# Performance work log

Measured on AMD Instinct MI355X. Metric: run time of the kernel, lower is better.

The kernel has to match this reference:

```python
import jax, jax.numpy as jnp
import numpy as np
import math

B, C, H, W = 8, 384, 14, 14
HEADS = 12
HC = C // HEADS
STRIDE = 2
K = 3
FACTOR = 2.0
rH = -(-H // STRIDE)
rW = -(-W // STRIDE)
N = H * W
S = rH * rW
KK = K * K
OFFSET_MAT = np.array([[0, -1], [-1, -1], [-1, 0], [-1, 1], [0, 1], [1, 1], [1, 0], [1, -1], [0, 0]], dtype=np.float32)


def bilinear_sample(img, coords):
    """img (Hi,Wi,C); coords (...,2) normalized (y,x) in [-1,1].
    Matches F.grid_sample(mode='bilinear', align_corners=True, padding_mode='zeros')."""
    Hi, Wi = img.shape[0], img.shape[1]
    py = (coords[..., 0] + 1.0) * 0.5 * (Hi - 1)
    px = (coords[..., 1] + 1.0) * 0.5 * (Wi - 1)
    y0 = jnp.floor(py)
    x0 = jnp.floor(px)
    wy1 = py - y0
    wx1 = px - x0

    def corner(yf, xf, wgt):
        valid = (yf >= 0) & (yf <= Hi - 1) & (xf >= 0) & (xf <= Wi - 1)
        yi = jnp.clip(yf, 0, Hi - 1).astype(jnp.int32)
        xi = jnp.clip(xf, 0, Wi - 1).astype(jnp.int32)
        return img[yi, xi] * (wgt * valid)[..., None]

    return (corner(y0, x0, (1 - wy1) * (1 - wx1)) + corner(y0, x0 + 1, (1 - wy1) * wx1)
            + corner(y0 + 1, x0, wy1 * (1 - wx1)) + corner(y0 + 1, x0 + 1, wy1 * wx1))


def _forward(x, Wq, bq, Wk, bk, Wv, bv, Wo1, bo1, Wdw, bdw, ln_g, ln_b, Wo2, Wco, posembed, Wp, bp):
    dt = x.dtype
    xh = jnp.transpose(x, (0, 2, 3, 1))                       # B,H,W,C
    q = jnp.einsum('bhwc,oc->bhwo', xh, Wq) + bq              # q_conv (1x1)

    # ---- offset network: 1x1 conv -> GELU -> 3x3 dw stride conv -> LN -> GELU -> 1x1 ----
    t = jax.nn.gelu(jnp.einsum('bhwc,oc->bhwo', q, Wo1) + bo1, approximate=False)
    ker = jnp.transpose(Wdw, (2, 3, 1, 0))                    # (3,3,1,C) for HWIO depthwise
    t = jax.lax.conv_general_dilated(t, ker, (STRIDE, STRIDE), ((1, 1), (1, 1)),
                                     dimension_numbers=('NHWC', 'HWIO', 'NHWC'),
                                     feature_group_count=C) + bdw  # B,rH,rW,C
    mu = t.mean(-1, keepdims=True)
    var = ((t - mu) ** 2).mean(-1, keepdims=True)
    t = (t - mu) / jnp.sqrt(var + 1e-5) * ln_g + ln_b
    t = jax.nn.gelu(t, approximate=False)
    off = jnp.einsum('bhwc,oc->bhwo', t, Wo2)                 # B,rH,rW,2*N ; channel = (g,h,w)
    off = off.reshape(B, rH, rW, 2, N)
    off = jnp.transpose(off, (0, 3, 4, 1, 2))                 # B,2,N,rH,rW
    ranges = jnp.array([1.0 / H, 1.0 / W], dtype=dt)
    off = jnp.tanh(off) * ranges[None, :, None, None, None] * FACTOR
    off = jnp.transpose(off, (0, 2, 3, 4, 1))                 # B,N,rH,rW,2 (y,x)

    # ---- strided reference grid + deformable bilinear gather from x ----
    gy = jnp.arange(0, H, STRIDE, dtype=dt) / (H - 1) * 2 - 1
    gx = jnp.arange(0, W, STRIDE, dtype=dt) / (W - 1) * 2 - 1
    ref = jnp.stack(jnp.meshgrid(gy, gx, indexing='ij'), -1)  # rH,rW,2
    dpos = off + ref
    sampled = jax.vmap(bilinear_sample)(xh, dpos).reshape(B, N, S, C)

    # ---- k x k center points with learned offsets ----
    cy = jnp.arange(H, dtype=dt)
    cx = jnp.arange(W, dtype=dt)
    center = jnp.stack(jnp.meshgrid(cy, cx, indexing='ij'), -1).reshape(N, 1, 2)
    offmat = jnp.asarray(OFFSET_MAT, dtype=dt)
    cpt = center + offmat[None]                               # N,KK,2
    cpt_norm = jnp.stack([jnp.clip(cpt[..., 0], 0, H) / (H - 1) * 2 - 1,
                          jnp.clip(cpt[..., 1], 0, W) / (W - 1) * 2 - 1], -1).reshape(N, K, K, 2)
    q_tok = q.reshape(B, N, C)
    co = jnp.tanh(jnp.einsum('bnc,oc->bno', q_tok, Wco).reshape(B, N, K, K, 2)) * ranges
    cgrid = co + cpt_norm[None]
    csampled = jax.vmap(bilinear_sample)(xh, cgrid).reshape(B, N, KK, C)

    feats = jnp.concatenate([sampled, csampled], axis=2)      # B,N,S+KK,C
    k = (jnp.einsum('bnsc,oc->bnso', feats, Wk) + bk).reshape(B, N, S + KK, HEADS, HC)
    v = (jnp.einsum('bnsc,oc->bnso', feats, Wv) + bv).reshape(B, N, S + KK, HEADS, HC)
    qh = q_tok.reshape(B, N, HEADS, HC)
    attn = jnp.einsum('bnhd,bnshd->bhns', qh, k)              # qk_scale=None -> no scaling

    # ---- dynamic relative position bias (grid_sample into rel-pos table) ----
    a = jnp.arange(0, H, STRIDE, dtype=dt)
    bcol = jnp.arange(0, W, dtype=dt)
    ref_pos = a[None, :] - bcol[:, None]                      # (W, rH)
    ref_pos_x = jnp.tile(ref_pos, (H, rH))                    # (N, S)
    ref_pos_y = jnp.repeat(jnp.repeat(ref_pos, W, axis=0), rW, axis=1)
    rpp = jnp.stack([ref_pos_y / (H - 1), ref_pos_x / (W - 1)], -1)  # N,S,2
    rel = rpp.reshape(N, rH, rW, 2)[None] - off               # B,N,rH,rW,2
    table = jnp.transpose(posembed, (1, 2, 0))                # (2H-1, 2W-1, heads)
    d_rel = bilinear_sample(table, rel).reshape(B, N, S, HEADS)
    cpt_raw = jnp.broadcast_to(center, (N, KK, 2)).reshape(N, K, K, 2)
    crel = co - cpt_raw[None]
    d_crel = bilinear_sample(table, crel).reshape(B, N, KK, HEADS)
    bias = jnp.concatenate([d_rel, d_crel], axis=2)           # B,N,S+KK,heads
    attn = attn + jnp.transpose(bias, (0, 3, 1, 2))
    attn = jax.nn.softmax(attn, axis=-1)

    out = jnp.einsum('bhns,bnshd->bnhd', attn, v).reshape(B, N, C)
    out = jnp.einsum('bnc,oc->bno', out, Wp) + bp             # proj (1x1)
    return jnp.transpose(out.reshape(B, H, W, C), (0, 3, 1, 2))


def setup_inputs() -> dict:
    key = jax.random.key(0)
    ks = jax.random.split(key, 20)
    def w(k, shape, s=0.05):
        return jax.random.normal(k, shape, dtype=jnp.float32) * s
    return {
        'x': jax.random.normal(ks[0], (B, C, H, W), dtype=jnp.float32),
        'Wq': w(ks[1], (C, C)), 'bq': w(ks[2], (C,)),
        'Wk': w(ks[3], (C, C)), 'bk': w(ks[4], (C,)),
        'Wv': w(ks[5], (C, C)), 'bv': w(ks[6], (C,)),
        'Wo1': w(ks[7], (C, C)), 'bo1': w(ks[8], (C,)),
        'Wdw': w(ks[9], (C, 1, 3, 3), 0.2), 'bdw': w(ks[10], (C,)),
        'ln_g': jnp.ones((C,), jnp.float32), 'ln_b': jnp.zeros((C,), jnp.float32),
        'Wo2': w(ks[11], (2 * N, C)),
        'Wco': w(ks[12], (2 * K * K, C)),
        'posembed': w(ks[13], (HEADS, 2 * H - 1, 2 * W - 1), 0.02),
        'Wp': w(ks[14], (C, C)), 'bp': w(ks[15], (C,)),
    }


def reference(x, Wq, bq, Wk, bk, Wv, bv, Wo1, bo1, Wdw, bdw, ln_g, ln_b, Wo2, Wco, posembed, Wp, bp):
    return _forward(x, Wq, bq, Wk, bk, Wv, bv, Wo1, bo1, Wdw, bdw, ln_g, ln_b, Wo2, Wco, posembed, Wp, bp)
```

## Files before the change

### kernel.cpp

```cpp
#include <hip/hip_runtime.h>
#include <hip/hip_bf16.h>
#include <math.h>

#define BB 8
#define CC 384
#define HH 14
#define WW 14
#define NHEADS 12
#define RH 7
#define RW 7
#define NN 196
#define SS 49
#define KKK 9
#define SK 58
#define TH 27
#define NTOK 1568
#define WSZ 147456
#define WO2SZ 150528

typedef float    f4 __attribute__((ext_vector_type(4)));
typedef _Float16 h8 __attribute__((ext_vector_type(8)));
typedef _Float16 h4 __attribute__((ext_vector_type(4)));

__device__ __forceinline__ float geluf(float x){ return 0.5f*x*(1.0f+erff(x*0.7071067811865475f)); }
__device__ __forceinline__ f4 mfma16h(h8 a, h8 b, f4 c){
  return __builtin_amdgcn_mfma_f32_16x16x32_f16(a, b, c, 0, 0, 0);
}

__constant__ float c_offm[9][2] = {{0,-1},{-1,-1},{-1,0},{-1,1},{0,1},{1,1},{1,0},{1,-1},{0,0}};

__global__ void __launch_bounds__(256) k_pre(const float* __restrict__ x,
    _Float16* __restrict__ xhh, _Float16* __restrict__ xlo,
    const float* __restrict__ Wq, const float* __restrict__ Wk, const float* __restrict__ Wo1,
    const float* __restrict__ Wp, const float* __restrict__ Wv, const float* __restrict__ Wo2,
    _Float16* __restrict__ Wh, _Float16* __restrict__ Wl){
  __shared__ float tile[48*203];
  int bid = blockIdx.x;
  int t = threadIdx.x;
  if (bid < 64){
    int b = bid >> 3, c0 = (bid & 7)*48;
    for (int i = t; i < 48*49; i += 256){
      int row = i / 49, seg = i % 49;
      f4 v = *(const f4*)(x + ((size_t)(b*CC + c0 + row))*NN + seg*4);
      #pragma unroll
      for (int j = 0; j < 4; ++j) tile[row*203 + seg*4 + j] = v[j];
    }
    __syncthreads();
    for (int i = t; i < 196*12; i += 256){
      int n = i / 12, seg = i % 12;
      h4 vh, vl;
      #pragma unroll
      for (int j = 0; j < 4; ++j){
        float v = tile[(seg*4 + j)*203 + n];
        vh[j] = (_Float16)v;
        vl[j] = (_Float16)(v - (float)vh[j]);
      }
      size_t o = ((size_t)(b*NN + n))*CC + c0 + seg*4;
      *(h4*)(xhh + o) = vh;
      *(h4*)(xlo + o) = vl;
    }
  } else if (bid < 424){
    int bid2 = bid - 64;
    int mat = bid2 / 72;
    int e0 = (bid2 % 72)*2048 + t*8;
    const float* src = mat==0?Wq: mat==1?Wk: mat==2?Wo1: mat==3?Wp: Wv;
    f4 v0 = *(const f4*)(src + e0);
    f4 v1 = *(const f4*)(src + e0 + 4);
    h8 hi, lo;
    #pragma unroll
    for (int j = 0; j < 4; ++j){
      hi[j]   = (_Float16)v0[j]; lo[j]   = (_Float16)(v0[j] - (float)hi[j]);
      hi[4+j] = (_Float16)v1[j]; lo[4+j] = (_Float16)(v1[j] - (float)hi[4+j]);
    }
    *(h8*)(Wh + (size_t)mat*WSZ + e0) = hi;
    *(h8*)(Wl + (size_t)mat*WSZ + e0) = lo;
  } else {
    int e0 = (bid - 424)*2048 + t*8;
    if (e0 < WO2SZ){
      f4 v0 = *(const f4*)(Wo2 + e0);
      f4 v1 = *(const f4*)(Wo2 + e0 + 4);
      h8 hi, lo;
      #pragma unroll
      for (int j = 0; j < 4; ++j){
        hi[j]   = (_Float16)v0[j]; lo[j]   = (_Float16)(v0[j] - (float)hi[j]);
        hi[4+j] = (_Float16)v1[j]; lo[4+j] = (_Float16)(v1[j] - (float)hi[4+j]);
      }
      *(h8*)(Wh + (size_t)5*WSZ + e0) = hi;
      *(h8*)(Wl + (size_t)5*WSZ + e0) = lo;
    }
  }
}

__device__ __forceinline__ void gemm_pre_body(
    const _Float16* __restrict__ Ahg, const _Float16* __restrict__ Alg,
    const _Float16* __restrict__ Bhg, const _Float16* __restrict__ Blg,
    int arow, int brow, _Float16* sbuf, int t, f4 acc[4]){
  _Float16* Ah = sbuf; _Float16* Al = sbuf + 2560;
  _Float16* Bh = sbuf + 5120; _Float16* Bl = sbuf + 7680;
  int w = t>>6, lane = t&63, col = lane&15, quad = lane>>4;
  int r = t>>2, cg = t&3;
  const _Float16* Arh = Ahg + (size_t)arow*384 + cg*8;
  const _Float16* Arl = Alg + (size_t)arow*384 + cg*8;
  const _Float16* Brh = Bhg + (size_t)brow*384 + cg*8;
  const _Float16* Brl = Blg + (size_t)brow*384 + cg*8;
  h8 ah = *(const h8*)(Arh), al = *(const h8*)(Arl);
  h8 bh = *(const h8*)(Brh), bl = *(const h8*)(Brl);
  for (int k0 = 0; k0 < 384; k0 += 32){
    __syncthreads();
    *(h8*)(Ah + r*40 + cg*8) = ah; *(h8*)(Al + r*40 + cg*8) = al;
    *(h8*)(Bh + r*40 + cg*8) = bh; *(h8*)(Bl + r*40 + cg*8) = bl;
    __syncthreads();
    if (k0 < 352){
      ah = *(const h8*)(Arh + k0 + 32); al = *(const h8*)(Arl + k0 + 32);
      bh = *(const h8*)(Brh + k0 + 32); bl = *(const h8*)(Brl + k0 + 32);
    }
    h8 afh = *(const h8*)(Ah + (w*16+col)*40 + quad*8);
    h8 afl = *(const h8*)(Al + (w*16+col)*40 + quad*8);
    #pragma unroll
    for (int nt = 0; nt < 4; ++nt){
      h8 bfh = *(const h8*)(Bh + (nt*16+col)*40 + quad*8);
      h8 bfl = *(const h8*)(Bl + (nt*16+col)*40 + quad*8);
      acc[nt] = mfma16h(afh, bfh, acc[nt]);
      acc[nt] = mfma16h(afl, bfh, acc[nt]);
      acc[nt] = mfma16h(afh, bfl, acc[nt]);
    }
  }
}

__global__ void __launch_bounds__(256) k_qkv(
    const _Float16* __restrict__ xhh, const _Float16* __restrict__ xlo,
    const _Float16* __restrict__ Wh, const _Float16* __restrict__ Wl,
    const float* __restrict__ bq,
    float* __restrict__ qf, _Float16* __restrict__ qfh, _Float16* __restrict__ qfl,
    _Float16* __restrict__ K2h, _Float16* __restrict__ VprojT){
  __shared__ __align__(16) _Float16 sbuf[10240];
  int t = threadIdx.x;
  int w = t>>6, lane = t&63, col = lane&15, quad = lane>>4;
  int bid = blockIdx.x;

  if (bid < 300){
    int isK = (bid >= 150) ? 1 : 0;
    int r2 = isK ? bid - 150 : bid;
    const _Float16* Bh = Wh + (size_t)(isK ? 1 : 0)*WSZ;
    const _Float16* Bl = Wl + (size_t)(isK ? 1 : 0)*WSZ;
    int m0 = (r2/6)*64, n0 = (r2%6)*64;
    int r = t>>2;
    int arow = min(m0 + r, NTOK-1);
    int brow = n0 + r;
    f4 acc[4] = {{0,0,0,0},{0,0,0,0},{0,0,0,0},{0,0,0,0}};
    gemm_pre_body(xhh, xlo, Bh, Bl, arow, brow, sbuf, t, acc);
    #pragma unroll
    for (int nt = 0; nt < 4; ++nt){
      #pragma unroll
      for (int rr = 0; rr < 4; ++rr){
        int m = m0 + w*16 + quad*4 + rr;
        int o = n0 + nt*16 + col;
        if (m >= NTOK) continue;
        if (isK){
          K2h[(size_t)m*384 + o] = (_Float16)acc[nt][rr];
        } else {
          float v = acc[nt][rr] + bq[o];
          qf[(size_t)m*384 + o] = v;
          _Float16 vh = (_Float16)v;
          qfh[(size_t)m*384 + o] = vh;
          qfl[(size_t)m*384 + o] = (_Float16)(v - (float)vh);
        }
      }
    }
  } else {
    int idx = bid - 300;
    int mo = idx % 6;
    int ny = (idx / 6) % 4;
    int b  = idx / 24;
    int m0 = mo*64, n0 = ny*64;
    int orow = m0 + w*16 + col;
    const _Float16* wvh = Wh + (size_t)4*WSZ + (size_t)orow*384;
    const _Float16* wvl = Wl + (size_t)4*WSZ + (size_t)orow*384;
    f4 acc[4] = {{0,0,0,0},{0,0,0,0},{0,0,0,0},{0,0,0,0}};
    for (int kt = 0; kt < 12; ++kt){
      h8 ah = *(const h8*)(wvh + kt*32 + quad*8);
      h8 al = *(const h8*)(wvl + kt*32 + quad*8);
      #pragma unroll
      for (int nt = 0; nt < 4; ++nt){
        int i = min(n0 + nt*16 + col, 195);
        h8 b8 = *(const h8*)(xhh + ((size_t)(b*196 + i))*384 + kt*32 + quad*8);
        acc[nt] = mfma16h(ah, b8, acc[nt]);
        acc[nt] = mfma16h(al, b8, acc[nt]);
      }
    }
    #pragma unroll
    for (int nt = 0; nt < 4; ++nt){
      #pragma unroll
      for (int rr = 0; rr < 4; ++rr){
        int o = m0 + w*16 + quad*4 + rr;
        int i = n0 + nt*16 + col;
        if (i < 224)
          VprojT[((size_t)(b*384 + o))*224 + i] = (i < 196) ? (_Float16)acc[nt][rr] : (_Float16)0.f;
      }
    }
  }
}

__global__ void __launch_bounds__(256) k_mid(
    const _Float16* __restrict__ qfh, const _Float16* __restrict__ qfl,
    const _Float16* __restrict__ Wh, const _Float16* __restrict__ Wl,
    const float* __restrict__ bo1, float* __restrict__ t1,
    const _Float16* __restrict__ K2h, _Float16* __restrict__ G16){
  __shared__ __align__(16) _Float16 sbuf[10240];
  int t = threadIdx.x;
  int w = t>>6, lane = t&63, col = lane&15, quad = lane>>4;
  int bid = blockIdx.x;
  if (bid < 150){
    const _Float16* Bh = Wh + (size_t)2*WSZ;
    const _Float16* Bl = Wl + (size_t)2*WSZ;
    int m0 = (bid/6)*64, n0 = (bid%6)*64;
    int r = t>>2;
    int arow = min(m0 + r, NTOK-1);
    int brow = n0 + r;
    f4 acc[4] = {{0,0,0,0},{0,0,0,0},{0,0,0,0},{0,0,0,0}};
    gemm_pre_body(qfh, qfl, Bh, Bl, arow, brow, sbuf, t, acc);
    #pragma unroll
    for (int nt = 0; nt < 4; ++nt){
      #pragma unroll
      for (int rr = 0; rr < 4; ++rr){
        int m = m0 + w*16 + quad*4 + rr;
        int o = n0 + nt*16 + col;
        if (m >= NTOK) continue;
        t1[(size_t)m*384 + o] = geluf(acc[nt][rr] + bo1[o]);
      }
    }
  } else {
    int idx = bid - 150;
    int m0 = (idx & 3)*64;
    int bh = idx >> 2; int b = bh / 12, h = bh - b*12;
    const _Float16* qr = qfh + ((size_t)(b*196 + min(m0 + w*16 + col, 195)))*384 + h*32;
    h8 a8 = *(const h8*)(qr + quad*8);
    f4 acc[13];
    #pragma unroll
    for (int nt = 0; nt < 13; ++nt){
      int i = min(nt*16 + col, 195);
      h8 b8 = *(const h8*)(K2h + ((size_t)(b*196 + i))*384 + h*32 + quad*8);
      f4 z = {0.f,0.f,0.f,0.f};
      acc[nt] = mfma16h(a8, b8, z);
    }
    #pragma unroll
    for (int nt = 0; nt < 13; ++nt){
      #pragma unroll
      for (int r = 0; r < 4; ++r){
        int m = m0 + w*16 + quad*4 + r;
        int i = nt*16 + col;
        if (m < 196 && i < 196)
          G16[((size_t)(b*196 + m))*2352 + h*196 + i] = (_Float16)acc[nt][r];
      }
    }
  }
}

__global__ void __launch_bounds__(384) k_dwln(const float* __restrict__ t1,
      const float* __restrict__ Wdw, const float* __restrict__ bdw,
      const float* __restrict__ lng, const float* __restrict__ lnb,
      _Float16* __restrict__ t2h, _Float16* __restrict__ t2l){
  int blk = blockIdx.x;
  int ow = blk % RW; int oh = (blk / RW) % RH; int b = blk / (RH*RW);
  int c = threadIdx.x;
  float acc = bdw[c];
  #pragma unroll
  for (int kh = 0; kh < 3; ++kh){
    int ih = oh*2 - 1 + kh;
    if (ih < 0 || ih >= HH) continue;
    #pragma unroll
    for (int kw = 0; kw < 3; ++kw){
      int iw = ow*2 - 1 + kw;
      if (iw < 0 || iw >= WW) continue;
      acc += t1[((b*HH + ih)*WW + iw)*CC + c] * Wdw[c*9 + kh*3 + kw];
    }
  }
  __shared__ float red[6];
  __shared__ float s_mu, s_rv;
  float v = acc;
  #pragma unroll
  for (int o = 32; o > 0; o >>= 1) v += __shfl_down(v, o);
  int wid = c >> 6, lane = c & 63;
  if (lane == 0) red[wid] = v;
  __syncthreads();
  if (c == 0){ float s = 0.f; for (int i = 0; i < 6; ++i) s += red[i]; s_mu = s / CC; }
  __syncthreads();
  float mu = s_mu;
  float d = acc - mu;
  v = d*d;
  #pragma unroll
  for (int o = 32; o > 0; o >>= 1) v += __shfl_down(v, o);
  if (lane == 0) red[wid] = v;
  __syncthreads();
  if (c == 0){ float s = 0.f; for (int i = 0; i < 6; ++i) s += red[i]; s_rv = rsqrtf(s / CC + 1e-5f); }
  __syncthreads();
  float val = geluf(d * s_rv * lng[c] + lnb[c]);
  _Float16 vh = (_Float16)val;
  t2h[blk*CC + c] = vh;
  t2l[blk*CC + c] = (_Float16)(val - (float)vh);
}

__global__ void __launch_bounds__(256) k_off(
    const _Float16* __restrict__ t2h, const _Float16* __restrict__ t2l,
    const _Float16* __restrict__ Wh, const _Float16* __restrict__ Wl,
    float* __restrict__ offp){
  __shared__ __align__(16) _Float16 sbuf[10240];
  int t = threadIdx.x;
  int w = t>>6, lane = t&63, col = lane&15, quad = lane>>4;
  int bid = blockIdx.x;
  int m0 = (bid/7)*64, n0 = (bid%7)*64;
  int r = t>>2;
  int arow = min(m0 + r, 391);
  int brow = min(n0 + r, 391);
  const _Float16* Bh = Wh + (size_t)5*WSZ;
  const _Float16* Bl = Wl + (size_t)5*WSZ;
  f4 acc[4] = {{0,0,0,0},{0,0,0,0},{0,0,0,0},{0,0,0,0}};
  gemm_pre_body(t2h, t2l, Bh, Bl, arow, brow, sbuf, t, acc);
  #pragma unroll
  for (int nt = 0; nt < 4; ++nt){
    #pragma unroll
    for (int rr = 0; rr < 4; ++rr){
      int row = m0 + w*16 + quad*4 + rr;
      int o = n0 + nt*16 + col;
      if (row < 392 && o < 392){
        int g = o / NN, nn = o % NN;
        int b = row / SS, s = row % SS;
        float rng = (g == 0) ? (1.0f/HH) : (1.0f/WW);
        offp[((b*NN + nn)*SS + s)*2 + g] = tanhf(acc[nt][rr]) * rng * 2.0f;
      }
    }
  }
}

__global__ void __launch_bounds__(256, 7) k_fused(
    const float* __restrict__ qf, const float* __restrict__ off,
    const _Float16* __restrict__ G16,
    const float* __restrict__ bk, const float* __restrict__ Wco, const float* __restrict__ pos,
    _Float16* __restrict__ agg16){
  __shared__ __align__(16) _Float16 Gs[2352];
  __shared__ __align__(16) float agg[12*228];
  __shared__ float scoreS[696];
  __shared__ float offl[98];
  __shared__ float colb[18];
  __shared__ float qbv[12];
  __shared__ uint2 tapv[232];
  float* qrow = agg;

  int blk = blockIdx.x;
  int n = blk % NN, b = blk / NN;
  int iy = n / WW, ix = n % WW;
  int t = threadIdx.x;

  {
    const h8* g8 = (const h8*)(G16 + (size_t)blk*2352);
    h8* gs8 = (h8*)Gs;
    for (int i = t; i < 294; i += 256) gs8[i] = g8[i];
  }
  {
    const f4* q4 = (const f4*)(qf + (size_t)blk*384);
    f4* qr4 = (f4*)qrow;
    for (int i = t; i < 96; i += 256) qr4[i] = q4[i];
  }
  for (int i = t; i < 98; i += 256) offl[i] = off[(size_t)blk*98 + i];
  __syncthreads();

  if (t < 144){
    int o = t >> 3, l = t & 7;
    const float* wr = Wco + o*384 + l*48;
    const float* qr = qrow + l*48;
    f4 a4 = {0.f,0.f,0.f,0.f};
    #pragma unroll
    for (int c = 0; c < 48; c += 4) a4 += (*(const f4*)(qr + c)) * (*(const f4*)(wr + c));
    float acc = a4[0]+a4[1]+a4[2]+a4[3];
    acc += __shfl_xor(acc, 1); acc += __shfl_xor(acc, 2); acc += __shfl_xor(acc, 4);
    if (l == 0){
      int g = o & 1;
      float range = (g == 0) ? (1.0f/HH) : (1.0f/WW);
      colb[o] = tanhf(acc) * range;
    }
  }
  if (t >= 160){
    int o = t - 160;
    int h = o >> 3, l = o & 7;
    float acc = 0.f;
    for (int d = l; d < 32; d += 8) acc += qrow[h*32 + d] * bk[h*32 + d];
    acc += __shfl_xor(acc, 1); acc += __shfl_xor(acc, 2); acc += __shfl_xor(acc, 4);
    if (l == 0 && h < 12) qbv[h] = acc;
  }
  __syncthreads();

  if (t < SK){
    float cy, cx;
    if (t < SS){
      int sy = t / RW, sx = t % RW;
      cy = offl[t*2+0] + ((2.0f*sy)/13.0f*2.0f - 1.0f);
      cx = offl[t*2+1] + ((2.0f*sx)/13.0f*2.0f - 1.0f);
    } else {
      int kk = t - SS;
      float cyr = fminf(fmaxf((float)iy + c_offm[kk][0], 0.f), (float)HH);
      float cxr = fminf(fmaxf((float)ix + c_offm[kk][1], 0.f), (float)WW);
      cy = colb[kk*2+0] + (cyr/13.0f*2.0f - 1.0f);
      cx = colb[kk*2+1] + (cxr/13.0f*2.0f - 1.0f);
    }
    float py = (cy + 1.0f)*0.5f*13.0f;
    float px = (cx + 1.0f)*0.5f*13.0f;
    float y0 = floorf(py), x0 = floorf(px);
    float wy1 = py - y0, wx1 = px - x0;
    #pragma unroll
    for (int k4 = 0; k4 < 4; ++k4){
      float yf = y0 + (k4 >> 1), xf = x0 + (k4 & 1);
      bool valid = (yf >= 0.f) && (yf <= 13.f) && (xf >= 0.f) && (xf <= 13.f);
      int yi = (int)fminf(fmaxf(yf, 0.f), 13.f);
      int xi = (int)fminf(fmaxf(xf, 0.f), 13.f);
      float wgt = ((k4 >> 1) ? wy1 : (1.f - wy1)) * ((k4 & 1) ? wx1 : (1.f - wx1));
      tapv[t*4 + k4] = make_uint2(__float_as_uint(valid ? wgt : 0.f),
                                  (unsigned)(yi*WW + xi));
    }
  }
  __syncthreads();
  for (int i = t; i < 12*228; i += 256) agg[i] = 0.f;

  if (t < 232){
    int s = t >> 2, grp = t & 3;
    float ry, rx;
    if (s < SS){
      int sy = s / RW, sx = s % RW;
      ry = (2.0f*sy - iy)/13.0f - offl[s*2+0];
      rx = (2.0f*sx - ix)/13.0f - offl[s*2+1];
    } else {
      int kk = s - SS;
      ry = colb[kk*2+0] - (float)iy;
      rx = colb[kk*2+1] - (float)ix;
    }
    float py = (ry + 1.0f)*0.5f*26.0f;
    float px = (rx + 1.0f)*0.5f*26.0f;
    float y0 = floorf(py), x0 = floorf(px);
    float wy1 = py - y0, wx1 = px - x0;
    int pidx[4]; float pw[4];
    #pragma unroll
    for (int k4 = 0; k4 < 4; ++k4){
      float yf = y0 + (k4 >> 1), xf = x0 + (k4 & 1);
      bool valid = (yf >= 0.f) && (yf <= 26.f) && (xf >= 0.f) && (xf <= 26.f);
      int yi = (int)fminf(fmaxf(yf, 0.f), 26.f);
      int xi = (int)fminf(fmaxf(xf, 0.f), 26.f);
      pidx[k4] = yi*TH + xi;
      float wgt = ((k4 >> 1) ? wy1 : (1.f - wy1)) * ((k4 & 1) ? wx1 : (1.f - wx1));
      pw[k4] = valid ? wgt : 0.f;
    }
    uint2 tp0 = tapv[s*4+0], tp1 = tapv[s*4+1], tp2 = tapv[s*4+2], tp3 = tapv[s*4+3];
    float tw0 = __uint_as_float(tp0.x), tw1 = __uint_as_float(tp1.x);
    float tw2 = __uint_as_float(tp2.x), tw3 = __uint_as_float(tp3.x);
    #pragma unroll
    for (int hh = 0; hh < 3; ++hh){
      int h = grp*3 + hh;
      const float* pt = pos + h*729;
      float val = qbv[h];
      val += pt[pidx[0]]*pw[0];
      val += pt[pidx[1]]*pw[1];
      val += pt[pidx[2]]*pw[2];
      val += pt[pidx[3]]*pw[3];
      const _Float16* gh = Gs + h*196;
      val += tw0*(float)gh[(int)tp0.y];
      val += tw1*(float)gh[(int)tp1.y];
      val += tw2*(float)gh[(int)tp2.y];
      val += tw3*(float)gh[(int)tp3.y];
      scoreS[h*58 + s] = val;
    }
  }
  __syncthreads();

  if (t < 192){
    int h = t >> 4, l = t & 15;
    float v[4];
    #pragma unroll
    for (int k = 0; k < 4; ++k){ int s = l + 16*k; v[k] = (s < SK) ? scoreS[h*58 + s] : -1e30f; }
    float mx = fmaxf(fmaxf(v[0], v[1]), fmaxf(v[2], v[3]));
    mx = fmaxf(mx, __shfl_xor(mx, 1)); mx = fmaxf(mx, __shfl_xor(mx, 2));
    mx = fmaxf(mx, __shfl_xor(mx, 4)); mx = fmaxf(mx, __shfl_xor(mx, 8));
    float e[4], sum = 0.f;
    #pragma unroll
    for (int k = 0; k < 4; ++k){ int s = l + 16*k; e[k] = (s < SK) ? expf(v[k] - mx) : 0.f; sum += e[k]; }
    sum += __shfl_xor(sum, 1); sum += __shfl_xor(sum, 2);
    sum += __shfl_xor(sum, 4); sum += __shfl_xor(sum, 8);
    float inv = 1.0f / sum;
    #pragma unroll
    for (int k = 0; k < 4; ++k){
      int s = l + 16*k;
      if (s < SK) scoreS[h*58 + s] = e[k]*inv;
    }
  }
  __syncthreads();

  if (t < 232){
    uint2 tp = tapv[t];
    float wv = __uint_as_float(tp.x);
    if (wv != 0.f){
      int s = t >> 2, cell = (int)tp.y;
      float* ag = agg + cell;
      #pragma unroll
      for (int h = 0; h < 12; ++h)
        atomicAdd(ag + h*228, scoreS[h*58 + s]*wv);
    }
  }
  __syncthreads();

  {
    _Float16* ar = agg16 + (size_t)blk*2688;
    for (int i = t; i < 336; i += 256){
      int d = i*8;
      int h = d / 224, j = d - h*224;
      const float* src = agg + h*228 + j;
      f4 a = *(const f4*)src;
      f4 c = *(const f4*)(src + 4);
      h8 o;
      #pragma unroll
      for (int k = 0; k < 4; ++k){ o[k] = (_Float16)a[k]; o[4+k] = (_Float16)c[k]; }
      *(h8*)(ar + d) = o;
    }
  }
}

__global__ void __launch_bounds__(256) k_av(const _Float16* __restrict__ agg16,
                                            const _Float16* __restrict__ VprojT,
                                            const float* __restrict__ bv,
                                            _Float16* __restrict__ otokh, _Float16* __restrict__ otokl){
  int t = threadIdx.x;
  int w = t>>6, lane = t&63, col = lane&15, quad = lane>>4;
  int m0 = blockIdx.x*64;
  int bh = blockIdx.y; int b = bh / 12, h = bh - b*12;
  const _Float16* ar = agg16 + ((size_t)(b*196 + min(m0 + w*16 + col, 195)))*2688 + h*224;
  f4 acc[2] = {{0,0,0,0},{0,0,0,0}};
  for (int kt = 0; kt < 7; ++kt){
    h8 a8 = *(const h8*)(ar + kt*32 + quad*8);
    #pragma unroll
    for (int nt = 0; nt < 2; ++nt){
      int o = h*32 + nt*16 + col;
      h8 b8 = *(const h8*)(VprojT + ((size_t)(b*384 + o))*224 + kt*32 + quad*8);
      acc[nt] = mfma16h(a8, b8, acc[nt]);
    }
  }
  #pragma unroll
  for (int nt = 0; nt < 2; ++nt){
    #pragma unroll
    for (int rr = 0; rr < 4; ++rr){
      int m = m0 + w*16 + quad*4 + rr;
      if (m < 196){
        int o = h*32 + nt*16 + col;
        float v = acc[nt][rr] + bv[o];
        size_t idx = ((size_t)(b*196 + m))*384 + o;
        _Float16 vh = (_Float16)v;
        otokh[idx] = vh;
        otokl[idx] = (_Float16)(v - (float)vh);
      }
    }
  }
}

__global__ void __launch_bounds__(256) k_proj(
    const _Float16* __restrict__ otokh, const _Float16* __restrict__ otokl,
    const _Float16* __restrict__ Wh, const _Float16* __restrict__ Wl,
    const float* __restrict__ bias, float* __restrict__ out){
  __shared__ __align__(16) _Float16 sbuf[10240];
  int t = threadIdx.x;
  int w = t>>6, lane = t&63, col = lane&15, quad = lane>>4;
  int m0 = blockIdx.x*64, n0 = blockIdx.y*64;
  int r = t>>2;
  int arow = min(m0 + r, NTOK-1);
  int brow = n0 + r;
  const _Float16* Bh = Wh + (size_t)3*WSZ;
  const _Float16* Bl = Wl + (size_t)3*WSZ;
  f4 acc[4] = {{0,0,0,0},{0,0,0,0},{0,0,0,0},{0,0,0,0}};
  gemm_pre_body(otokh, otokl, Bh, Bl, arow, brow, sbuf, t, acc);
  float* tile = (float*)sbuf;
  __syncthreads();
  #pragma unroll
  for (int nt = 0; nt < 4; ++nt)
    #pragma unroll
    for (int rr = 0; rr < 4; ++rr)
      tile[(w*16 + quad*4 + rr)*65 + nt*16 + col] = acc[nt][rr];
  __syncthreads();
  for (int i = t; i < 1024; i += 256){
    int o_l = i >> 4, ms = i & 15;
    int m = m0 + ms*4;
    if (m >= NTOK) continue;
    int bb = m / NN, nnn = m % NN;
    int o = n0 + o_l;
    float bo = bias[o];
    f4 v = { tile[(ms*4+0)*65 + o_l] + bo, tile[(ms*4+1)*65 + o_l] + bo,
             tile[(ms*4+2)*65 + o_l] + bo, tile[(ms*4+3)*65 + o_l] + bo };
    *(f4*)(out + ((size_t)bb*384 + o)*NN + nnn) = v;
  }
}

extern "C" void kernel_launch(void* const* d_in, const int* in_sizes, int n_in,
                              void* d_out, int out_size, void* d_ws, size_t ws_size,
                              hipStream_t stream){
  const float* x    = (const float*)d_in[0];
  const float* Wq   = (const float*)d_in[1];
  const float* bq   = (const float*)d_in[2];
  const float* Wk   = (const float*)d_in[3];
  const float* bk   = (const float*)d_in[4];
  const float* Wv   = (const float*)d_in[5];
  const float* bv   = (const float*)d_in[6];
  const float* Wo1  = (const float*)d_in[7];
  const float* bo1  = (const float*)d_in[8];
  const float* Wdw  = (const float*)d_in[9];
  const float* bdw  = (const float*)d_in[10];
  const float* ln_g = (const float*)d_in[11];
  const float* ln_b = (const float*)d_in[12];
  const float* Wo2  = (const float*)d_in[13];
  const float* Wco  = (const float*)d_in[14];
  const float* pos  = (const float*)d_in[15];
  const float* Wp   = (const float*)d_in[16];
  const float* bp   = (const float*)d_in[17];
  float* out = (float*)d_out;

  float* ws   = (float*)d_ws;
  float* qf   = ws;
  float* t1   = qf   + 602112;
  float* offp = t1   + 602112;
  _Float16* xhh    = (_Float16*)(offp + 153664);
  _Float16* xlo    = xhh    + 602112;
  _Float16* qfh    = xlo    + 602112;
  _Float16* qfl    = qfh    + 602112;
  _Float16* t2h    = qfl    + 602112;
  _Float16* t2l    = t2h    + 150528;
  _Float16* K2h    = t2l    + 150528;
  _Float16* VprojT = K2h    + 602112;
  _Float16* otokh  = VprojT + 688128;
  _Float16* otokl  = otokh  + 602112;
  _Float16* Wh     = otokl  + 602112;
  _Float16* Wl     = Wh     + 5*WSZ + WO2SZ;
  _Float16* G16    = Wl     + 5*WSZ + WO2SZ;
  _Float16* agg16  = G16    + 3687936;

  k_pre<<<498, 256, 0, stream>>>(x, xhh, xlo, Wq, Wk, Wo1, Wp, Wv, Wo2, Wh, Wl);
  k_qkv<<<492, 256, 0, stream>>>(xhh, xlo, Wh, Wl, bq, qf, qfh, qfl, K2h, VprojT);
  k_mid<<<534, 256, 0, stream>>>(qfh, qfl, Wh, Wl, bo1, t1, K2h, G16);
  k_dwln<<<392, 384, 0, stream>>>(t1, Wdw, bdw, ln_g, ln_b, t2h, t2l);
  k_off<<<49, 256, 0, stream>>>(t2h, t2l, Wh, Wl, offp);
  k_fused<<<1568, 256, 0, stream>>>(qf, offp, G16, bk, Wco, pos, agg16);
  k_av<<<dim3(4,96), 256, 0, stream>>>(agg16, VprojT, bv, otokh, otokl);
  k_proj<<<dim3(25,6), 256, 0, stream>>>(otokh, otokl, Wh, Wl, bp, out);
}
```

Baseline: 194.9 us.

## Fuse offset 1x1 conv with depthwise conv and LayerNorm into one kernel

Merges the Wo1 GEMM+GELU with the strided depthwise conv, LayerNorm and GELU into a single kernel. Each output position recomputes only the 9 input tokens its 3x3 window needs, using MFMA, and keeps them in LDS. This removes the t1 global round trip and one kernel launch. The cost is redundant GEMM work, since overlapping windows recompute shared tokens, and MFMA tiles where only 9 of 16 rows are used. The fused kernel also runs 384-thread blocks in which 128 threads sit idle for the G16 part.

```diff
diff --git a/kernel.cpp b/kernel.cpp
--- a/kernel.cpp
+++ b/kernel.cpp
@@ -201,38 +201,25 @@
   }
 }
 
-__global__ void __launch_bounds__(256) k_mid(
+__global__ void __launch_bounds__(384) k_mdw(
     const _Float16* __restrict__ qfh, const _Float16* __restrict__ qfl,
     const _Float16* __restrict__ Wh, const _Float16* __restrict__ Wl,
-    const float* __restrict__ bo1, float* __restrict__ t1,
-    const _Float16* __restrict__ K2h, _Float16* __restrict__ G16){
-  __shared__ __align__(16) _Float16 sbuf[10240];
+    const float* __restrict__ bo1,
+    const float* __restrict__ Wdw, const float* __restrict__ bdw,
+    const float* __restrict__ lng, const float* __restrict__ lnb,
+    const _Float16* __restrict__ K2h, _Float16* __restrict__ G16,
+    _Float16* __restrict__ t2h, _Float16* __restrict__ t2l){
+  __shared__ float ldsT1[16*388];
+  __shared__ float red[6];
+  __shared__ float s_mu, s_rv;
+  int bid = blockIdx.x;
   int t = threadIdx.x;
-  int w = t>>6, lane = t&63, col = lane&15, quad = lane>>4;
-  int bid = blockIdx.x;
-  if (bid < 150){
-    const _Float16* Bh = Wh + (size_t)2*WSZ;
-    const _Float16* Bl = Wl + (size_t)2*WSZ;
-    int m0 = (bid/6)*64, n0 = (bid%6)*64;
-    int r = t>>2;
-    int arow = min(m0 + r, NTOK-1);
-    int brow = n0 + r;
-    f4 acc[4] = {{0,0,0,0},{0,0,0,0},{0,0,0,0},{0,0,0,0}};
-    gemm_pre_body(qfh, qfl, Bh, Bl, arow, brow, sbuf, t, acc);
-    #pragma unroll
-    for (int nt = 0; nt < 4; ++nt){
-      #pragma unroll
-      for (int rr = 0; rr < 4; ++rr){
-        int m = m0 + w*16 + quad*4 + rr;
-        int o = n0 + nt*16 + col;
-        if (m >= NTOK) continue;
-        t1[(size_t)m*384 + o] = geluf(acc[nt][rr] + bo1[o]);
-      }
-    }
-  } else {
-    int idx = bid - 150;
-    int m0 = (idx & 3)*64;
-    int bh = idx >> 2; int b = bh / 12, h = bh - b*12;
+
+  if (bid < 384){
+    if (t >= 256) return;
+    int w = t>>6, lane = t&63, col = lane&15, quad = lane>>4;
+    int m0 = (bid & 3)*64;
+    int bh = bid >> 2; int b = bh / 12, h = bh - b*12;
     const _Float16* qr = qfh + ((size_t)(b*196 + min(m0 + w*16 + col, 195)))*384 + h*32;
     h8 a8 = *(const h8*)(qr + quad*8);
     f4 acc[13];
@@ -253,17 +240,59 @@
           G16[((size_t)(b*196 + m))*2352 + h*196 + i] = (_Float16)acc[nt][r];
       }
     }
-  }
-}
-
-__global__ void __launch_bounds__(384) k_dwln(const float* __restrict__ t1,
-      const float* __restrict__ Wdw, const float* __restrict__ bdw,
-      const float* __restrict__ lng, const float* __restrict__ lnb,
-      _Float16* __restrict__ t2h, _Float16* __restrict__ t2l){
-  int blk = blockIdx.x;
-  int ow = blk % RW; int oh = (blk / RW) % RH; int b = blk / (RH*RW);
-  int c = threadIdx.x;
-  float acc = bdw[c];
+    return;
+  }
+
+  int blk = bid - 384;
+  int ow = blk % RW, oh = (blk / RW) % RH, b = blk / (RH*RW);
+
+  if (t < 256){
+    int w = t>>6, lane = t&63, col = lane&15, quad = lane>>4;
+    int r = col;
+    int tok;
+    if (r < 9){
+      int ih = oh*2 - 1 + r/3;
+      int iw = ow*2 - 1 + r%3;
+      tok = b*196 + min(max(ih,0),13)*14 + min(max(iw,0),13);
+    } else {
+      tok = b*196;
+    }
+    const _Float16* aph = qfh + (size_t)tok*384 + quad*8;
+    const _Float16* apl = qfl + (size_t)tok*384 + quad*8;
+    h8 afh[12], afl[12];
+    #pragma unroll
+    for (int ks = 0; ks < 12; ++ks){
+      afh[ks] = *(const h8*)(aph + ks*32);
+      afl[ks] = *(const h8*)(apl + ks*32);
+    }
+    const _Float16* B1h = Wh + (size_t)2*WSZ;
+    const _Float16* B1l = Wl + (size_t)2*WSZ;
+    #pragma unroll
+    for (int nt = 0; nt < 6; ++nt){
+      int o = w*96 + nt*16 + col;
+      const _Float16* bph = B1h + (size_t)o*384 + quad*8;
+      const _Float16* bpl = B1l + (size_t)o*384 + quad*8;
+      f4 acc = {0.f,0.f,0.f,0.f};
+      #pragma unroll
+      for (int ks = 0; ks < 12; ++ks){
+        h8 bfh = *(const h8*)(bph + ks*32);
+        h8 bfl = *(const h8*)(bpl + ks*32);
+        acc = mfma16h(afh[ks], bfh, acc);
+        acc = mfma16h(afl[ks], bfh, acc);
+        acc = mfma16h(afh[ks], bfl, acc);
+      }
+      float bo = bo1[o];
+      #pragma unroll
+      for (int rr = 0; rr < 4; ++rr){
+        int row = quad*4 + rr;
+        if (row < 9) ldsT1[row*388 + o] = geluf(acc[rr] + bo);
+      }
+    }
+  }
+  __syncthreads();
+
+  int c = t;
+  float acc2 = bdw[c];
   #pragma unroll
   for (int kh = 0; kh < 3; ++kh){
     int ih = oh*2 - 1 + kh;
@@ -272,25 +301,23 @@
     for (int kw = 0; kw < 3; ++kw){
       int iw = ow*2 - 1 + kw;
       if (iw < 0 || iw >= WW) continue;
-      acc += t1[((b*HH + ih)*WW + iw)*CC + c] * Wdw[c*9 + kh*3 + kw];
-    }
-  }
-  __shared__ float red[6];
-  __shared__ float s_mu, s_rv;
-  float v = acc;
+      acc2 += ldsT1[(kh*3+kw)*388 + c] * Wdw[c*9 + kh*3 + kw];
+    }
+  }
+  float v = acc2;
   #pragma unroll
   for (int o = 32; o > 0; o >>= 1) v += __shfl_down(v, o);
-  int wid = c >> 6, lane = c & 63;
-  if (lane == 0) red[wid] = v;
+  int wid = c >> 6, lane2 = c & 63;
+  if (lane2 == 0) red[wid] = v;
   __syncthreads();
   if (c == 0){ float s = 0.f; for (int i = 0; i < 6; ++i) s += red[i]; s_mu = s / CC; }
   __syncthreads();
   float mu = s_mu;
-  float d = acc - mu;
+  float d = acc2 - mu;
   v = d*d;
   #pragma unroll
   for (int o = 32; o > 0; o >>= 1) v += __shfl_down(v, o);
-  if (lane == 0) red[wid] = v;
+  if (lane2 == 0) red[wid] = v;
   __syncthreads();
   if (c == 0){ float s = 0.f; for (int i = 0; i < 6; ++i) s += red[i]; s_rv = rsqrtf(s / CC + 1e-5f); }
   __syncthreads();
@@ -636,8 +663,7 @@
 
   k_pre<<<498, 256, 0, stream>>>(x, xhh, xlo, Wq, Wk, Wo1, Wp, Wv, Wo2, Wh, Wl);
   k_qkv<<<492, 256, 0, stream>>>(xhh, xlo, Wh, Wl, bq, qf, qfh, qfl, K2h, VprojT);
-  k_mid<<<534, 256, 0, stream>>>(qfh, qfl, Wh, Wl, bo1, t1, K2h, G16);
-  k_dwln<<<392, 384, 0, stream>>>(t1, Wdw, bdw, ln_g, ln_b, t2h, t2l);
+  k_mdw<<<776, 384, 0, stream>>>(qfh, qfl, Wh, Wl, bo1, Wdw, bdw, ln_g, ln_b, K2h, G16, t2h, t2l);
   k_off<<<49, 256, 0, stream>>>(t2h, t2l, Wh, Wl, offp);
   k_fused<<<1568, 256, 0, stream>>>(qf, offp, G16, bk, Wco, pos, agg16);
   k_av<<<dim3(4,96), 256, 0, stream>>>(agg16, VprojT, bv, otokh, otokl);
```

Result: slower. 232.3 us (+19.2%).
